# Kernel optimization log

Hardware: AMD Instinct MI355X
Metric: run time of the kernel (lower is better)

Reference implementation:

```python
import jax, jax.numpy as jnp
import numpy as np

KSIZE = 3  # module init kwarg


def setup_inputs() -> dict:
    key = jax.random.key(0)
    k1, k2, k3 = jax.random.split(key, 3)
    shape = (16, 3, 512, 512)  # [B, C, H, W]
    return {
        "sr": jax.random.normal(k1, shape, jnp.float32),
        "sr_ema": jax.random.normal(k2, shape, jnp.float32),
        "hr": jax.random.normal(k3, shape, jnp.float32),
    }


def _local_var(res, ksize):
    """Unbiased variance over a ksize x ksize sliding window with reflect pad.

    Matches torch: reflect-pad then unfold + var(unbiased=True). Implemented as a
    box-filter over sum and sum-of-squares (no ksize^2-larger unfold tensor).
    res: [B, 1, H, W] -> [B, 1, H, W]
    """
    pad = (ksize - 1) // 2
    rp = jnp.pad(res, ((0, 0), (0, 0), (pad, pad), (pad, pad)), mode="reflect")
    n = ksize * ksize
    win = (1, 1, ksize, ksize)
    strides = (1, 1, 1, 1)
    zero = jnp.zeros((), rp.dtype)
    s = jax.lax.reduce_window(rp, zero, jax.lax.add, win, strides, "VALID")
    sq = jax.lax.reduce_window(rp * rp, zero, jax.lax.add, win, strides, "VALID")
    # unbiased: (sum(x^2) - sum(x)^2/n) / (n-1)
    return (sq - s * s / n) / (n - 1)


def reference(sr, sr_ema, hr):
    # per-pixel channel-summed residuals, [B, 1, H, W]
    residual_ema = jnp.sum(jnp.abs(hr - sr_ema), axis=1, keepdims=True) / 255.0
    residual_sr = jnp.sum(jnp.abs(hr - sr), axis=1, keepdims=True) / 255.0

    r_det = jax.lax.stop_gradient(residual_sr)  # .clone().detach() in torch

    # patch-level weight: unbiased var over (C=1, H, W) per sample, ** (1/5)
    n_patch = r_det.shape[1] * r_det.shape[2] * r_det.shape[3]
    mean = jnp.mean(r_det, axis=(-1, -2, -3), keepdims=True)
    patch_var = jnp.sum((r_det - mean) ** 2, axis=(-1, -2, -3), keepdims=True) / (n_patch - 1)
    patch_w = patch_var ** 0.2  # [B,1,1,1]

    pixel_w = _local_var(r_det, KSIZE)  # [B,1,H,W]

    overall_w = patch_w * pixel_w
    overall_w = jnp.where(residual_sr < residual_ema, jnp.zeros((), overall_w.dtype), overall_w)

    # L1 loss (mean reduction) between weighted sr and weighted hr
    return jnp.mean(jnp.abs(overall_w * sr - overall_w * hr))
```

## Files before the change

### kernel.cpp

```cpp
#include <hip/hip_runtime.h>
#include <math.h>


#define BB 16
#define HH 512
#define WW 512
#define HW (HH * WW)
#define CHW (3 * HW)
#define STRIP 8
#define NSTRIPS (HH / STRIP)
#define REG_PER_B (2 * NSTRIPS)
#define NREGIONS (BB * REG_PER_B)
#define NBLOCKS (NREGIONS / 4)

__device__ __forceinline__ int reflect_h(int gh) {
  gh = gh < 0 ? -gh : gh;
  return gh >= HH ? 2 * HH - 2 - gh : gh;
}

struct Row {
  float4 r;
  float4 e;
  float lv, rv;
};

template <bool WITH_E>
__device__ __forceinline__ Row load_row(const float* __restrict__ hrb,
                                        const float* __restrict__ srb,
                                        const float* __restrict__ emb, int n,
                                        int col, int wedge, bool edge_lane,
                                        int lane) {
  Row o;
  const int gh = reflect_h(n);
  const float* hp = hrb + gh * WW + col;
  const float* sp = srb + gh * WW + col;
  float4 h0 = *(const float4*)hp;
  float4 h1 = *(const float4*)(hp + HW);
  float4 h2 = *(const float4*)(hp + 2 * HW);
  float4 s0 = *(const float4*)sp;
  float4 s1 = *(const float4*)(sp + HW);
  float4 s2 = *(const float4*)(sp + 2 * HW);
  o.r.x = (fabsf(h0.x - s0.x) + fabsf(h1.x - s1.x) + fabsf(h2.x - s2.x)) / 255.0f;
  o.r.y = (fabsf(h0.y - s0.y) + fabsf(h1.y - s1.y) + fabsf(h2.y - s2.y)) / 255.0f;
  o.r.z = (fabsf(h0.z - s0.z) + fabsf(h1.z - s1.z) + fabsf(h2.z - s2.z)) / 255.0f;
  o.r.w = (fabsf(h0.w - s0.w) + fabsf(h1.w - s1.w) + fabsf(h2.w - s2.w)) / 255.0f;
  if (WITH_E) {
    const float* ep = emb + gh * WW + col;
    float4 e0 = *(const float4*)ep;
    float4 e1 = *(const float4*)(ep + HW);
    float4 e2 = *(const float4*)(ep + 2 * HW);
    o.e.x = (fabsf(h0.x - e0.x) + fabsf(h1.x - e1.x) + fabsf(h2.x - e2.x)) / 255.0f;
    o.e.y = (fabsf(h0.y - e0.y) + fabsf(h1.y - e1.y) + fabsf(h2.y - e2.y)) / 255.0f;
    o.e.z = (fabsf(h0.z - e0.z) + fabsf(h1.z - e1.z) + fabsf(h2.z - e2.z)) / 255.0f;
    o.e.w = (fabsf(h0.w - e0.w) + fabsf(h1.w - e1.w) + fabsf(h2.w - e2.w)) / 255.0f;
  } else {
    o.e = make_float4(0.f, 0.f, 0.f, 0.f);
  }
  float edge = 0.f;
  if (edge_lane) {
    const float* hq = hrb + gh * WW + wedge;
    const float* sq = srb + gh * WW + wedge;
    edge = (fabsf(hq[0] - sq[0]) + fabsf(hq[HW] - sq[HW]) +
            fabsf(hq[2 * HW] - sq[2 * HW])) /
           255.0f;
  }
  float lvs = __shfl_up(o.r.w, 1, 64);
  float rvs = __shfl_down(o.r.x, 1, 64);
  o.lv = (lane == 0) ? edge : lvs;
  o.rv = (lane == 63) ? edge : rvs;
  return o;
}

__device__ __forceinline__ void row6(const Row& R, float* v) {
  v[0] = R.lv; v[1] = R.r.x; v[2] = R.r.y; v[3] = R.r.z; v[4] = R.r.w; v[5] = R.rv;
}

__global__ __launch_bounds__(256) void wl1_main(
    const float* __restrict__ sr, const float* __restrict__ srema,
    const float* __restrict__ hr, float* __restrict__ p_sum,
    float* __restrict__ p_sum2, float* __restrict__ p_loss) {
  const int tid = threadIdx.x;
  const int lane = tid & 63;
  const int region = blockIdx.x * 4 + (tid >> 6);
  const int b = region >> 7;
  const int rem = region & 127;
  const int w0 = (rem & 1) << 8;
  const int h0 = (rem >> 1) * STRIP;

  const float* __restrict__ srb = sr + (size_t)b * CHW;
  const float* __restrict__ hrb = hr + (size_t)b * CHW;
  const float* __restrict__ emb = srema + (size_t)b * CHW;

  const int col = w0 + 4 * lane;
  const int wl = (w0 == 0) ? 1 : w0 - 1;
  const int wrr = (w0 + 256 >= WW) ? (2 * WW - 2 - (w0 + 256)) : (w0 + 256);
  const bool edge_lane = (lane == 0) || (lane == 63);
  const int wedge = (lane == 0) ? wl : wrr;

  Row A = load_row<false>(hrb, srb, emb, h0 - 1, col, wedge, edge_lane, lane);
  Row B = load_row<true>(hrb, srb, emb, h0, col, wedge, edge_lane, lane);
  Row C = load_row<true>(hrb, srb, emb, h0 + 1, col, wedge, edge_lane, lane);

  float v1 = 0.f, v2 = 0.f, v3 = 0.f;
#pragma unroll
  for (int i = 0; i < STRIP; ++i) {
    Row D = C;
    if (i + 2 < STRIP) {
      D = load_row<true>(hrb, srb, emb, h0 + i + 2, col, wedge, edge_lane, lane);
    } else if (i + 2 == STRIP) {
      D = load_row<false>(hrb, srb, emb, h0 + i + 2, col, wedge, edge_lane, lane);
    }

    float vA[6], vB[6], vC[6];
    row6(A, vA); row6(B, vB); row6(C, vC);
    float cs[6], cq[6];
#pragma unroll
    for (int j = 0; j < 6; ++j) {
      cs[j] = vA[j] + vB[j] + vC[j];
      cq[j] = vA[j] * vA[j] + vB[j] * vB[j] + vC[j] * vC[j];
    }
    const float rcv[4] = {B.r.x, B.r.y, B.r.z, B.r.w};
    const float ev[4] = {B.e.x, B.e.y, B.e.z, B.e.w};
#pragma unroll
    for (int c = 0; c < 4; ++c) {
      float s = cs[c] + cs[c + 1] + cs[c + 2];
      float q = cq[c] + cq[c + 1] + cq[c + 2];
      float pvar = (q - s * s / 9.0f) / 8.0f;
      float rc = rcv[c];
      v1 += rc;
      v2 += rc * rc;
      if (rc >= ev[c]) v3 += pvar * (255.0f * rc);
    }
    A = B; B = C; C = D;
  }

#pragma unroll
  for (int off = 32; off > 0; off >>= 1) {
    v1 += __shfl_down(v1, off, 64);
    v2 += __shfl_down(v2, off, 64);
    v3 += __shfl_down(v3, off, 64);
  }
  if (lane == 0) {
    p_sum[region] = v1;
    p_sum2[region] = v2;
    p_loss[region] = v3;
  }
}

__global__ __launch_bounds__(1024) void wl1_reduce(
    const float* __restrict__ p_sum, const float* __restrict__ p_sum2,
    const float* __restrict__ p_loss, float* __restrict__ out) {
  const int tid = threadIdx.x;
  const int b = tid >> 6, k = tid & 63;
  double s = 0.0, s2 = 0.0, sl = 0.0;
#pragma unroll
  for (int j = 0; j < REG_PER_B; j += 64) {
    int i = b * REG_PER_B + j + k;
    s += (double)p_sum[i];
    s2 += (double)p_sum2[i];
    sl += (double)p_loss[i];
  }
#pragma unroll
  for (int off = 32; off > 0; off >>= 1) {
    s += __shfl_down(s, off, 64);
    s2 += __shfl_down(s2, off, 64);
    sl += __shfl_down(sl, off, 64);
  }
  __shared__ double acc[BB];
  if (k == 0) {
    const double n = (double)HW;
    double var = (s2 - s * s / n) / (n - 1.0);
    acc[b] = pow(var, 0.2) * sl;
  }
  __syncthreads();
  if (tid == 0) {
    double tot = 0.0;
#pragma unroll
    for (int j = 0; j < BB; ++j) tot += acc[j];
    out[0] = (float)(tot / (double)((size_t)BB * CHW));
  }
}

extern "C" void kernel_launch(void* const* d_in, const int* in_sizes, int n_in,
                              void* d_out, int out_size, void* d_ws,
                              size_t ws_size, hipStream_t stream) {
  const float* sr = (const float*)d_in[0];
  const float* srema = (const float*)d_in[1];
  const float* hr = (const float*)d_in[2];
  float* out = (float*)d_out;

  float* p_sum = (float*)d_ws;
  float* p_sum2 = p_sum + NREGIONS;
  float* p_loss = p_sum2 + NREGIONS;

  wl1_main<<<NBLOCKS, 256, 0, stream>>>(sr, srema, hr, p_sum, p_sum2, p_loss);
  wl1_reduce<<<1, 1024, 0, stream>>>(p_sum, p_sum2, p_loss, out);
}
```

Baseline: 173.4 us.

## Stage residual rows in shared memory and process 4-row full-width tiles per block

Replaces the per-wave register-rolling 8-row strip with blocks that each load a full-width tile of 6 residual rows (4 output rows plus halo) into LDS. Precomputed masked weights go into a second LDS array, and the 3x3 window is read from shared memory, so the cross-lane shuffles and separate edge-lane loads are gone. Halo reloads rise from 2 per 8 rows to 2 per 4 rows, which means more redundant global reads of sr and hr. In exchange there are more, smaller blocks, and a block-level reduction is added along with extra syncthreads and an occupancy hint.

Measured after the change: 163.7 us. -5.6%, faster.

```diff
diff --git a/kernel.cpp b/kernel.cpp
--- a/kernel.cpp
+++ b/kernel.cpp
@@ -7,131 +7,105 @@
 #define WW 512
 #define HW (HH * WW)
 #define CHW (3 * HW)
-#define STRIP 8
-#define NSTRIPS (HH / STRIP)
-#define REG_PER_B (2 * NSTRIPS)
-#define NREGIONS (BB * REG_PER_B)
-#define NBLOCKS (NREGIONS / 4)
+#define STRIPS 128
+#define NBLOCKS (BB * STRIPS)
+#define NREGIONS NBLOCKS
+#define REG_PER_B STRIPS
 
 __device__ __forceinline__ int reflect_h(int gh) {
   gh = gh < 0 ? -gh : gh;
   return gh >= HH ? 2 * HH - 2 - gh : gh;
 }
 
-struct Row {
-  float4 r;
-  float4 e;
-  float lv, rv;
-};
-
-template <bool WITH_E>
-__device__ __forceinline__ Row load_row(const float* __restrict__ hrb,
-                                        const float* __restrict__ srb,
-                                        const float* __restrict__ emb, int n,
-                                        int col, int wedge, bool edge_lane,
-                                        int lane) {
-  Row o;
-  const int gh = reflect_h(n);
-  const float* hp = hrb + gh * WW + col;
-  const float* sp = srb + gh * WW + col;
-  float4 h0 = *(const float4*)hp;
-  float4 h1 = *(const float4*)(hp + HW);
-  float4 h2 = *(const float4*)(hp + 2 * HW);
-  float4 s0 = *(const float4*)sp;
-  float4 s1 = *(const float4*)(sp + HW);
-  float4 s2 = *(const float4*)(sp + 2 * HW);
-  o.r.x = (fabsf(h0.x - s0.x) + fabsf(h1.x - s1.x) + fabsf(h2.x - s2.x)) / 255.0f;
-  o.r.y = (fabsf(h0.y - s0.y) + fabsf(h1.y - s1.y) + fabsf(h2.y - s2.y)) / 255.0f;
-  o.r.z = (fabsf(h0.z - s0.z) + fabsf(h1.z - s1.z) + fabsf(h2.z - s2.z)) / 255.0f;
-  o.r.w = (fabsf(h0.w - s0.w) + fabsf(h1.w - s1.w) + fabsf(h2.w - s2.w)) / 255.0f;
-  if (WITH_E) {
-    const float* ep = emb + gh * WW + col;
-    float4 e0 = *(const float4*)ep;
-    float4 e1 = *(const float4*)(ep + HW);
-    float4 e2 = *(const float4*)(ep + 2 * HW);
-    o.e.x = (fabsf(h0.x - e0.x) + fabsf(h1.x - e1.x) + fabsf(h2.x - e2.x)) / 255.0f;
-    o.e.y = (fabsf(h0.y - e0.y) + fabsf(h1.y - e1.y) + fabsf(h2.y - e2.y)) / 255.0f;
-    o.e.z = (fabsf(h0.z - e0.z) + fabsf(h1.z - e1.z) + fabsf(h2.z - e2.z)) / 255.0f;
-    o.e.w = (fabsf(h0.w - e0.w) + fabsf(h1.w - e1.w) + fabsf(h2.w - e2.w)) / 255.0f;
-  } else {
-    o.e = make_float4(0.f, 0.f, 0.f, 0.f);
-  }
-  float edge = 0.f;
-  if (edge_lane) {
-    const float* hq = hrb + gh * WW + wedge;
-    const float* sq = srb + gh * WW + wedge;
-    edge = (fabsf(hq[0] - sq[0]) + fabsf(hq[HW] - sq[HW]) +
-            fabsf(hq[2 * HW] - sq[2 * HW])) /
-           255.0f;
-  }
-  float lvs = __shfl_up(o.r.w, 1, 64);
-  float rvs = __shfl_down(o.r.x, 1, 64);
-  o.lv = (lane == 0) ? edge : lvs;
-  o.rv = (lane == 63) ? edge : rvs;
-  return o;
-}
-
-__device__ __forceinline__ void row6(const Row& R, float* v) {
-  v[0] = R.lv; v[1] = R.r.x; v[2] = R.r.y; v[3] = R.r.z; v[4] = R.r.w; v[5] = R.rv;
-}
-
-__global__ __launch_bounds__(256) void wl1_main(
+__global__ __launch_bounds__(256, 8) void wl1_main(
     const float* __restrict__ sr, const float* __restrict__ srema,
     const float* __restrict__ hr, float* __restrict__ p_sum,
     float* __restrict__ p_sum2, float* __restrict__ p_loss) {
+  __shared__ float rt[6][WW];
+  __shared__ float ft[4][WW];
   const int tid = threadIdx.x;
-  const int lane = tid & 63;
-  const int region = blockIdx.x * 4 + (tid >> 6);
-  const int b = region >> 7;
-  const int rem = region & 127;
-  const int w0 = (rem & 1) << 8;
-  const int h0 = (rem >> 1) * STRIP;
-
+  const int bid = blockIdx.x;
+  const int b = bid >> 7;
+  const int h0 = (bid & 127) << 2;
   const float* __restrict__ srb = sr + (size_t)b * CHW;
   const float* __restrict__ hrb = hr + (size_t)b * CHW;
   const float* __restrict__ emb = srema + (size_t)b * CHW;
 
-  const int col = w0 + 4 * lane;
-  const int wl = (w0 == 0) ? 1 : w0 - 1;
-  const int wrr = (w0 + 256 >= WW) ? (2 * WW - 2 - (w0 + 256)) : (w0 + 256);
-  const bool edge_lane = (lane == 0) || (lane == 63);
-  const int wedge = (lane == 0) ? wl : wrr;
+#pragma unroll
+  for (int it = 0; it < 3; ++it) {
+    const int item = it * 256 + tid;
+    const int row = item >> 7;
+    const int g = item & 127;
+    const int gh = reflect_h(h0 - 1 + row);
+    const float* hp = hrb + gh * WW + 4 * g;
+    const float* sp = srb + gh * WW + 4 * g;
+    float4 h0v = *(const float4*)hp;
+    float4 h1v = *(const float4*)(hp + HW);
+    float4 h2v = *(const float4*)(hp + 2 * HW);
+    float4 s0v = *(const float4*)sp;
+    float4 s1v = *(const float4*)(sp + HW);
+    float4 s2v = *(const float4*)(sp + 2 * HW);
+    float4 r4;
+    r4.x = (fabsf(h0v.x - s0v.x) + fabsf(h1v.x - s1v.x) + fabsf(h2v.x - s2v.x)) / 255.0f;
+    r4.y = (fabsf(h0v.y - s0v.y) + fabsf(h1v.y - s1v.y) + fabsf(h2v.y - s2v.y)) / 255.0f;
+    r4.z = (fabsf(h0v.z - s0v.z) + fabsf(h1v.z - s1v.z) + fabsf(h2v.z - s2v.z)) / 255.0f;
+    r4.w = (fabsf(h0v.w - s0v.w) + fabsf(h1v.w - s1v.w) + fabsf(h2v.w - s2v.w)) / 255.0f;
+    *(float4*)&rt[row][4 * g] = r4;
+    if (row >= 1 && row <= 4) {
+      const float* ep = emb + gh * WW + 4 * g;
+      float4 e0v = *(const float4*)ep;
+      float4 e1v = *(const float4*)(ep + HW);
+      float4 e2v = *(const float4*)(ep + 2 * HW);
+      float4 e4, f4;
+      e4.x = (fabsf(h0v.x - e0v.x) + fabsf(h1v.x - e1v.x) + fabsf(h2v.x - e2v.x)) / 255.0f;
+      e4.y = (fabsf(h0v.y - e0v.y) + fabsf(h1v.y - e1v.y) + fabsf(h2v.y - e2v.y)) / 255.0f;
+      e4.z = (fabsf(h0v.z - e0v.z) + fabsf(h1v.z - e1v.z) + fabsf(h2v.z - e2v.z)) / 255.0f;
+      e4.w = (fabsf(h0v.w - e0v.w) + fabsf(h1v.w - e1v.w) + fabsf(h2v.w - e2v.w)) / 255.0f;
+      f4.x = (r4.x >= e4.x) ? 255.0f * r4.x : 0.0f;
+      f4.y = (r4.y >= e4.y) ? 255.0f * r4.y : 0.0f;
+      f4.z = (r4.z >= e4.z) ? 255.0f * r4.z : 0.0f;
+      f4.w = (r4.w >= e4.w) ? 255.0f * r4.w : 0.0f;
+      *(float4*)&ft[row - 1][4 * g] = f4;
+    }
+  }
+  __syncthreads();
 
-  Row A = load_row<false>(hrb, srb, emb, h0 - 1, col, wedge, edge_lane, lane);
-  Row B = load_row<true>(hrb, srb, emb, h0, col, wedge, edge_lane, lane);
-  Row C = load_row<true>(hrb, srb, emb, h0 + 1, col, wedge, edge_lane, lane);
-
+  const int g = tid & 127;
+  const int r0 = tid >> 7;
+  const int li = (g == 0) ? 1 : 4 * g - 1;
+  const int ri = (g == 127) ? 510 : 4 * g + 4;
   float v1 = 0.f, v2 = 0.f, v3 = 0.f;
 #pragma unroll
-  for (int i = 0; i < STRIP; ++i) {
-    Row D = C;
-    if (i + 2 < STRIP) {
-      D = load_row<true>(hrb, srb, emb, h0 + i + 2, col, wedge, edge_lane, lane);
-    } else if (i + 2 == STRIP) {
-      D = load_row<false>(hrb, srb, emb, h0 + i + 2, col, wedge, edge_lane, lane);
+  for (int k = 0; k < 2; ++k) {
+    const int orow = r0 + 2 * k;
+    float cs[6] = {0, 0, 0, 0, 0, 0}, cq[6] = {0, 0, 0, 0, 0, 0};
+    float center[4];
+#pragma unroll
+    for (int dr = 0; dr < 3; ++dr) {
+      const int row = orow + dr;
+      float4 c4 = *(const float4*)&rt[row][4 * g];
+      float lv = rt[row][li];
+      float rv = rt[row][ri];
+      float v[6] = {lv, c4.x, c4.y, c4.z, c4.w, rv};
+#pragma unroll
+      for (int j = 0; j < 6; ++j) {
+        cs[j] += v[j];
+        cq[j] += v[j] * v[j];
+      }
+      if (dr == 1) { center[0] = c4.x; center[1] = c4.y; center[2] = c4.z; center[3] = c4.w; }
     }
-
-    float vA[6], vB[6], vC[6];
-    row6(A, vA); row6(B, vB); row6(C, vC);
-    float cs[6], cq[6];
-#pragma unroll
-    for (int j = 0; j < 6; ++j) {
-      cs[j] = vA[j] + vB[j] + vC[j];
-      cq[j] = vA[j] * vA[j] + vB[j] * vB[j] + vC[j] * vC[j];
-    }
-    const float rcv[4] = {B.r.x, B.r.y, B.r.z, B.r.w};
-    const float ev[4] = {B.e.x, B.e.y, B.e.z, B.e.w};
+    float4 f4 = *(const float4*)&ft[orow][4 * g];
+    const float fv[4] = {f4.x, f4.y, f4.z, f4.w};
 #pragma unroll
     for (int c = 0; c < 4; ++c) {
       float s = cs[c] + cs[c + 1] + cs[c + 2];
       float q = cq[c] + cq[c + 1] + cq[c + 2];
       float pvar = (q - s * s / 9.0f) / 8.0f;
-      float rc = rcv[c];
+      float rc = center[c];
       v1 += rc;
       v2 += rc * rc;
-      if (rc >= ev[c]) v3 += pvar * (255.0f * rc);
+      v3 += pvar * fv[c];
     }
-    A = B; B = C; C = D;
   }
 
 #pragma unroll
@@ -140,10 +114,18 @@
     v2 += __shfl_down(v2, off, 64);
     v3 += __shfl_down(v3, off, 64);
   }
+  __syncthreads();
+  const int wave = tid >> 6, lane = tid & 63;
   if (lane == 0) {
-    p_sum[region] = v1;
-    p_sum2[region] = v2;
-    p_loss[region] = v3;
+    rt[0][wave] = v1;
+    rt[0][8 + wave] = v2;
+    rt[0][16 + wave] = v3;
+  }
+  __syncthreads();
+  if (tid == 0) {
+    p_sum[bid] = rt[0][0] + rt[0][1] + rt[0][2] + rt[0][3];
+    p_sum2[bid] = rt[0][8] + rt[0][9] + rt[0][10] + rt[0][11];
+    p_loss[bid] = rt[0][16] + rt[0][17] + rt[0][18] + rt[0][19];
   }
 }
 
```

## Halve strip height and software-pipeline row loads with explicit issue/consume split

Applied to the files above, without the earlier changes.

Strip height drops from 8 to 4 rows, which doubles the region and block count. Row loading is split into an issue phase that only fetches raw values and a consume phase that computes residuals, so the next row's loads are in flight while the current row is processed. Edge handling is simplified per half: the outer image border reuses an in-lane value and only the inner seam lane loads extra columns. The mask and scale are folded into a per-row factor, and launch bounds now request 4 blocks per CU. The cost is more halo rows re-read per output row and extra register pressure from holding raw loads.

Result: slower. 231.9 us (+33.7%).

```diff
diff --git a/kernel.cpp b/kernel.cpp
--- a/kernel.cpp
+++ b/kernel.cpp
@@ -7,132 +7,145 @@
 #define WW 512
 #define HW (HH * WW)
 #define CHW (3 * HW)
-#define STRIP 8
-#define NSTRIPS (HH / STRIP)
-#define REG_PER_B (2 * NSTRIPS)
-#define NREGIONS (BB * REG_PER_B)
-#define NBLOCKS (NREGIONS / 4)
+#define NREGIONS 4096
+#define REG_PER_B 256
+#define NBLOCKS 1024
 
 __device__ __forceinline__ int reflect_h(int gh) {
   gh = gh < 0 ? -gh : gh;
   return gh >= HH ? 2 * HH - 2 - gh : gh;
 }
 
-struct Row {
-  float4 r;
-  float4 e;
-  float lv, rv;
+struct Raw {
+  float4 h0, h1, h2, s0, s1, s2;
+  float4 m0, m1, m2;
+  float eh0, eh1, eh2, es0, es1, es2;
 };
 
-template <bool WITH_E>
-__device__ __forceinline__ Row load_row(const float* __restrict__ hrb,
-                                        const float* __restrict__ srb,
-                                        const float* __restrict__ emb, int n,
-                                        int col, int wedge, bool edge_lane,
-                                        int lane) {
-  Row o;
+__device__ __forceinline__ void issue_row(Raw& R, int n, bool withE,
+                                          const float* __restrict__ hrb,
+                                          const float* __restrict__ srb,
+                                          const float* __restrict__ emb,
+                                          int col, int ecol, bool edge_lane) {
   const int gh = reflect_h(n);
   const float* hp = hrb + gh * WW + col;
   const float* sp = srb + gh * WW + col;
-  float4 h0 = *(const float4*)hp;
-  float4 h1 = *(const float4*)(hp + HW);
-  float4 h2 = *(const float4*)(hp + 2 * HW);
-  float4 s0 = *(const float4*)sp;
-  float4 s1 = *(const float4*)(sp + HW);
-  float4 s2 = *(const float4*)(sp + 2 * HW);
-  o.r.x = (fabsf(h0.x - s0.x) + fabsf(h1.x - s1.x) + fabsf(h2.x - s2.x)) / 255.0f;
-  o.r.y = (fabsf(h0.y - s0.y) + fabsf(h1.y - s1.y) + fabsf(h2.y - s2.y)) / 255.0f;
-  o.r.z = (fabsf(h0.z - s0.z) + fabsf(h1.z - s1.z) + fabsf(h2.z - s2.z)) / 255.0f;
-  o.r.w = (fabsf(h0.w - s0.w) + fabsf(h1.w - s1.w) + fabsf(h2.w - s2.w)) / 255.0f;
-  if (WITH_E) {
-    const float* ep = emb + gh * WW + col;
-    float4 e0 = *(const float4*)ep;
-    float4 e1 = *(const float4*)(ep + HW);
-    float4 e2 = *(const float4*)(ep + 2 * HW);
-    o.e.x = (fabsf(h0.x - e0.x) + fabsf(h1.x - e1.x) + fabsf(h2.x - e2.x)) / 255.0f;
-    o.e.y = (fabsf(h0.y - e0.y) + fabsf(h1.y - e1.y) + fabsf(h2.y - e2.y)) / 255.0f;
-    o.e.z = (fabsf(h0.z - e0.z) + fabsf(h1.z - e1.z) + fabsf(h2.z - e2.z)) / 255.0f;
-    o.e.w = (fabsf(h0.w - e0.w) + fabsf(h1.w - e1.w) + fabsf(h2.w - e2.w)) / 255.0f;
+  R.h0 = *(const float4*)hp;
+  R.h1 = *(const float4*)(hp + HW);
+  R.h2 = *(const float4*)(hp + 2 * HW);
+  R.s0 = *(const float4*)sp;
+  R.s1 = *(const float4*)(sp + HW);
+  R.s2 = *(const float4*)(sp + 2 * HW);
+  if (withE) {
+    const float* mp = emb + gh * WW + col;
+    R.m0 = *(const float4*)mp;
+    R.m1 = *(const float4*)(mp + HW);
+    R.m2 = *(const float4*)(mp + 2 * HW);
+  }
+  if (edge_lane) {
+    const float* hq = hrb + gh * WW + ecol;
+    const float* sq = srb + gh * WW + ecol;
+    R.eh0 = hq[0]; R.eh1 = hq[HW]; R.eh2 = hq[2 * HW];
+    R.es0 = sq[0]; R.es1 = sq[HW]; R.es2 = sq[2 * HW];
+  }
+}
+
+__device__ __forceinline__ void consume_row(const Raw& R, bool withE,
+                                            bool half1, int lane, float* v6,
+                                            float4* f4out) {
+  float4 r;
+  r.x = (fabsf(R.h0.x - R.s0.x) + fabsf(R.h1.x - R.s1.x) + fabsf(R.h2.x - R.s2.x)) / 255.0f;
+  r.y = (fabsf(R.h0.y - R.s0.y) + fabsf(R.h1.y - R.s1.y) + fabsf(R.h2.y - R.s2.y)) / 255.0f;
+  r.z = (fabsf(R.h0.z - R.s0.z) + fabsf(R.h1.z - R.s1.z) + fabsf(R.h2.z - R.s2.z)) / 255.0f;
+  r.w = (fabsf(R.h0.w - R.s0.w) + fabsf(R.h1.w - R.s1.w) + fabsf(R.h2.w - R.s2.w)) / 255.0f;
+  float er = (fabsf(R.eh0 - R.es0) + fabsf(R.eh1 - R.es1) + fabsf(R.eh2 - R.es2)) / 255.0f;
+  float lvs = __shfl_up(r.w, 1, 64);
+  float rvs = __shfl_down(r.x, 1, 64);
+  float lv, rv;
+  if (half1) {
+    lv = (lane == 0) ? er : lvs;
+    rv = (lane == 63) ? r.z : rvs;
   } else {
-    o.e = make_float4(0.f, 0.f, 0.f, 0.f);
-  }
-  float edge = 0.f;
-  if (edge_lane) {
-    const float* hq = hrb + gh * WW + wedge;
-    const float* sq = srb + gh * WW + wedge;
-    edge = (fabsf(hq[0] - sq[0]) + fabsf(hq[HW] - sq[HW]) +
-            fabsf(hq[2 * HW] - sq[2 * HW])) /
-           255.0f;
-  }
-  float lvs = __shfl_up(o.r.w, 1, 64);
-  float rvs = __shfl_down(o.r.x, 1, 64);
-  o.lv = (lane == 0) ? edge : lvs;
-  o.rv = (lane == 63) ? edge : rvs;
-  return o;
-}
-
-__device__ __forceinline__ void row6(const Row& R, float* v) {
-  v[0] = R.lv; v[1] = R.r.x; v[2] = R.r.y; v[3] = R.r.z; v[4] = R.r.w; v[5] = R.rv;
-}
-
-__global__ __launch_bounds__(256) void wl1_main(
+    lv = (lane == 0) ? r.y : lvs;
+    rv = (lane == 63) ? er : rvs;
+  }
+  v6[0] = lv; v6[1] = r.x; v6[2] = r.y; v6[3] = r.z; v6[4] = r.w; v6[5] = rv;
+  if (withE) {
+    float4 e;
+    e.x = (fabsf(R.h0.x - R.m0.x) + fabsf(R.h1.x - R.m1.x) + fabsf(R.h2.x - R.m2.x)) / 255.0f;
+    e.y = (fabsf(R.h0.y - R.m0.y) + fabsf(R.h1.y - R.m1.y) + fabsf(R.h2.y - R.m2.y)) / 255.0f;
+    e.z = (fabsf(R.h0.z - R.m0.z) + fabsf(R.h1.z - R.m1.z) + fabsf(R.h2.z - R.m2.z)) / 255.0f;
+    e.w = (fabsf(R.h0.w - R.m0.w) + fabsf(R.h1.w - R.m1.w) + fabsf(R.h2.w - R.m2.w)) / 255.0f;
+    f4out->x = (r.x >= e.x) ? 255.0f * r.x : 0.0f;
+    f4out->y = (r.y >= e.y) ? 255.0f * r.y : 0.0f;
+    f4out->z = (r.z >= e.z) ? 255.0f * r.z : 0.0f;
+    f4out->w = (r.w >= e.w) ? 255.0f * r.w : 0.0f;
+  }
+}
+
+__device__ __forceinline__ void stencil(const float* rU, const float* rM,
+                                        const float* rD, const float4 f,
+                                        float& v1, float& v2, float& v3) {
+  float cs[6], cq[6];
+#pragma unroll
+  for (int j = 0; j < 6; ++j) {
+    cs[j] = rU[j] + rM[j] + rD[j];
+    cq[j] = rU[j] * rU[j] + rM[j] * rM[j] + rD[j] * rD[j];
+  }
+  const float fv[4] = {f.x, f.y, f.z, f.w};
+#pragma unroll
+  for (int c = 0; c < 4; ++c) {
+    float s = cs[c] + cs[c + 1] + cs[c + 2];
+    float q = cq[c] + cq[c + 1] + cq[c + 2];
+    float pvar = (q - s * s / 9.0f) / 8.0f;
+    float rc = rM[c + 1];
+    v1 += rc;
+    v2 += rc * rc;
+    v3 += pvar * fv[c];
+  }
+}
+
+__global__ __launch_bounds__(256, 4) void wl1_main(
     const float* __restrict__ sr, const float* __restrict__ srema,
     const float* __restrict__ hr, float* __restrict__ p_sum,
     float* __restrict__ p_sum2, float* __restrict__ p_loss) {
   const int tid = threadIdx.x;
   const int lane = tid & 63;
   const int region = blockIdx.x * 4 + (tid >> 6);
-  const int b = region >> 7;
-  const int rem = region & 127;
-  const int w0 = (rem & 1) << 8;
-  const int h0 = (rem >> 1) * STRIP;
-
+  const int b = region >> 8;
+  const int rem = region & 255;
+  const int half = rem & 1;
+  const int h0 = (rem >> 1) << 2;
+  const int w0 = half << 8;
   const float* __restrict__ srb = sr + (size_t)b * CHW;
   const float* __restrict__ hrb = hr + (size_t)b * CHW;
   const float* __restrict__ emb = srema + (size_t)b * CHW;
-
   const int col = w0 + 4 * lane;
-  const int wl = (w0 == 0) ? 1 : w0 - 1;
-  const int wrr = (w0 + 256 >= WW) ? (2 * WW - 2 - (w0 + 256)) : (w0 + 256);
-  const bool edge_lane = (lane == 0) || (lane == 63);
-  const int wedge = (lane == 0) ? wl : wrr;
-
-  Row A = load_row<false>(hrb, srb, emb, h0 - 1, col, wedge, edge_lane, lane);
-  Row B = load_row<true>(hrb, srb, emb, h0, col, wedge, edge_lane, lane);
-  Row C = load_row<true>(hrb, srb, emb, h0 + 1, col, wedge, edge_lane, lane);
-
+  const bool half1 = (half != 0);
+  const int ecol = half1 ? 255 : 256;
+  const bool edge_lane = half1 ? (lane == 0) : (lane == 63);
+
+  Raw A, B;
+  float r0[6], r1[6], r2[6], r3[6], r4[6], r5[6];
+  float4 f0, f1, f2, f3, fd;
   float v1 = 0.f, v2 = 0.f, v3 = 0.f;
-#pragma unroll
-  for (int i = 0; i < STRIP; ++i) {
-    Row D = C;
-    if (i + 2 < STRIP) {
-      D = load_row<true>(hrb, srb, emb, h0 + i + 2, col, wedge, edge_lane, lane);
-    } else if (i + 2 == STRIP) {
-      D = load_row<false>(hrb, srb, emb, h0 + i + 2, col, wedge, edge_lane, lane);
-    }
-
-    float vA[6], vB[6], vC[6];
-    row6(A, vA); row6(B, vB); row6(C, vC);
-    float cs[6], cq[6];
-#pragma unroll
-    for (int j = 0; j < 6; ++j) {
-      cs[j] = vA[j] + vB[j] + vC[j];
-      cq[j] = vA[j] * vA[j] + vB[j] * vB[j] + vC[j] * vC[j];
-    }
-    const float rcv[4] = {B.r.x, B.r.y, B.r.z, B.r.w};
-    const float ev[4] = {B.e.x, B.e.y, B.e.z, B.e.w};
-#pragma unroll
-    for (int c = 0; c < 4; ++c) {
-      float s = cs[c] + cs[c + 1] + cs[c + 2];
-      float q = cq[c] + cq[c + 1] + cq[c + 2];
-      float pvar = (q - s * s / 9.0f) / 8.0f;
-      float rc = rcv[c];
-      v1 += rc;
-      v2 += rc * rc;
-      if (rc >= ev[c]) v3 += pvar * (255.0f * rc);
-    }
-    A = B; B = C; C = D;
-  }
+
+  issue_row(A, h0 - 1, false, hrb, srb, emb, col, ecol, edge_lane);
+  issue_row(B, h0 + 0, true, hrb, srb, emb, col, ecol, edge_lane);
+  consume_row(A, false, half1, lane, r0, &fd);
+  issue_row(A, h0 + 1, true, hrb, srb, emb, col, ecol, edge_lane);
+  consume_row(B, true, half1, lane, r1, &f0);
+  issue_row(B, h0 + 2, true, hrb, srb, emb, col, ecol, edge_lane);
+  consume_row(A, true, half1, lane, r2, &f1);
+  stencil(r0, r1, r2, f0, v1, v2, v3);
+  issue_row(A, h0 + 3, true, hrb, srb, emb, col, ecol, edge_lane);
+  consume_row(B, true, half1, lane, r3, &f2);
+  stencil(r1, r2, r3, f1, v1, v2, v3);
+  issue_row(B, h0 + 4, false, hrb, srb, emb, col, ecol, edge_lane);
+  consume_row(A, true, half1, lane, r4, &f3);
+  stencil(r2, r3, r4, f2, v1, v2, v3);
+  consume_row(B, false, half1, lane, r5, &fd);
+  stencil(r3, r4, r5, f3, v1, v2, v3);
 
 #pragma unroll
   for (int off = 32; off > 0; off >>= 1) {
```
